# Performance work log

Hardware: AMD Instinct MI355X
Metric: run time of the kernel (lower is better)

The kernel has to match this reference:

```python
import jax, jax.numpy as jnp
import numpy as np

NUM_HEADS = 6
HEAD_SIZE = 64
N_EMBD = 384


def setup_inputs() -> dict:
    key = jax.random.key(0)
    ks = jax.random.split(key, 6)
    B, T, C = 4, 2048, N_EMBD
    D = NUM_HEADS * HEAD_SIZE  # 384
    x = jax.random.normal(ks[0], (B, T, C), dtype=jnp.float32)
    scale = 1.0 / np.sqrt(C)
    Wq = jax.random.normal(ks[1], (C, D), dtype=jnp.float32) * scale
    Wk = jax.random.normal(ks[2], (C, D), dtype=jnp.float32) * scale
    Wv = jax.random.normal(ks[3], (C, D), dtype=jnp.float32) * scale
    Wp = jax.random.normal(ks[4], (D, N_EMBD), dtype=jnp.float32) * scale
    bp = jnp.zeros((N_EMBD,), dtype=jnp.float32)
    return {"x": x, "Wq": Wq, "Wk": Wk, "Wv": Wv, "Wp": Wp, "bp": bp}


def reference(x, Wq, Wk, Wv, Wp, bp):
    B, T, C = x.shape
    H, Dh = NUM_HEADS, HEAD_SIZE
    # QKV projections (no bias), split into heads: [B, H, T, Dh]
    q = (x @ Wq).reshape(B, T, H, Dh).transpose(0, 2, 1, 3)
    k = (x @ Wk).reshape(B, T, H, Dh).transpose(0, 2, 1, 3)
    v = (x @ Wv).reshape(B, T, H, Dh).transpose(0, 2, 1, 3)
    # scaled dot-product scores [B, H, T, T]
    scores = jnp.einsum("bhqd,bhkd->bhqk", q, k) / jnp.sqrt(jnp.float32(Dh))
    causal = jnp.tril(jnp.ones((T, T), dtype=bool))
    scores = jnp.where(causal, scores, jnp.float32(-1e9))
    attn = jax.nn.softmax(scores, axis=-1)
    # dropout is identity at inference (Keras Dropout inactive outside training)
    out = jnp.einsum("bhqk,bhkd->bhqd", attn, v)
    out = out.transpose(0, 2, 1, 3).reshape(B, T, H * Dh)
    return out @ Wp + bp
```

## Files before the change

kernel.cpp:

```cpp
#include <hip/hip_runtime.h>
#include <hip/hip_bf16.h>

typedef __bf16 bf16x8 __attribute__((ext_vector_type(8)));
typedef float floatx4 __attribute__((ext_vector_type(4)));
typedef unsigned short us4 __attribute__((ext_vector_type(4)));
typedef unsigned short us8 __attribute__((ext_vector_type(8)));
typedef unsigned short ushort_t;

#define MFMA(a,b,c) __builtin_amdgcn_mfma_f32_16x16x32_bf16((a),(b),(c),0,0,0)


__device__ __forceinline__ ushort_t f2bf(float f){
  unsigned u = __builtin_bit_cast(unsigned, f);
  u = u + 0x7fffu + ((u>>16)&1u);
  return (ushort_t)(u>>16);
}

__device__ __forceinline__ us4 pack4(float4 a){
  us4 o;
  o[0]=f2bf(a.x); o[1]=f2bf(a.y); o[2]=f2bf(a.z); o[3]=f2bf(a.w);
  return o;
}

__device__ __forceinline__ us4 cvt4(floatx4 v){
  union { us4 s; __hip_bfloat162 h[2]; } u;
  float2 t;
  t.x=v[0]; t.y=v[1]; u.h[0]=__float22bfloat162_rn(t);
  t.x=v[2]; t.y=v[3]; u.h[1]=__float22bfloat162_rn(t);
  return u.s;
}

__global__ __launch_bounds__(256) void prep(
    const float* __restrict__ x,
    const float* __restrict__ w0, const float* __restrict__ w1,
    const float* __restrict__ w2, const float* __restrict__ w3,
    ushort_t* __restrict__ xb,
    ushort_t* __restrict__ wt_qkv, ushort_t* __restrict__ wt_p){
  __shared__ ushort_t tile[64][65];
  int bx = blockIdx.x;
  if (bx < 3072){
    int i = (bx*256 + threadIdx.x)*4;
    int row = i/384, col = i - row*384;
    float4 v = *(const float4*)(x + i);
    us4 o;
    o[0]=f2bf(v.x); o[1]=f2bf(v.y); o[2]=f2bf(v.z); o[3]=f2bf(v.w);
    *(us4*)(xb + ((row>>4)*48 + (col>>3))*128 + (row&15)*8 + (col&7)) = o;
    return;
  }
  int t6 = bx - 3072;
  int z = t6/36, rem = t6%36, by = rem/6, bxx = rem%6;
  const float* src; ushort_t* dst;
  if      (z==0){ src=w0; dst=wt_qkv;             }
  else if (z==1){ src=w1; dst=wt_qkv + 147456;    }
  else if (z==2){ src=w2; dst=wt_qkv + 2*147456;  }
  else          { src=w3; dst=wt_p;               }
  int r0 = by*64, c0 = bxx*64;
  int t = threadIdx.x, r = t>>2, cs = (t&3)*16;
  #pragma unroll
  for (int i=0;i<16;i++) tile[r][cs+i] = f2bf(src[(r0+r)*384 + c0+cs+i]);
  __syncthreads();
  int n = c0 + r, t16n = n>>4, rn = n&15;
  int k0 = r0 + cs;
  #pragma unroll
  for (int i=0;i<16;i++){
    int k = k0 + i;
    dst[(t16n*48 + (k>>3))*128 + rn*8 + (k&7)] = tile[cs+i][r];
  }
}

__global__ __launch_bounds__(64) void qkv_gemm(
    const ushort_t* __restrict__ x, const ushort_t* __restrict__ wt,
    ushort_t* __restrict__ qb, ushort_t* __restrict__ kb, ushort_t* __restrict__ vtb){
  __shared__ ushort_t tr[16*72];
  int lane = threadIdx.x&63, l15 = lane&15, quad = lane>>4;
  int mb = blockIdx.x*64, mt = blockIdx.x*4;
  int z  = blockIdx.y/6;
  int nt16 = (blockIdx.y - z*6)*4;
  int n0 = nt16*16;
  const ushort_t* wbase = wt + z*147456;
  floatx4 acc[4][4];
  #pragma unroll
  for (int qs=0;qs<4;qs++)
    #pragma unroll
    for (int nt=0;nt<4;nt++) acc[qs][nt]=(floatx4){0,0,0,0};
  #pragma unroll
  for (int kt=0; kt<12; kt++){
    bf16x8 a[4], b[4];
    #pragma unroll
    for (int qs=0; qs<4; qs++)
      a[qs] = *(const bf16x8*)(x + ((mt+qs)*48 + kt*4+quad)*128 + l15*8);
    #pragma unroll
    for (int nt=0; nt<4; nt++)
      b[nt] = *(const bf16x8*)(wbase + ((nt16+nt)*48 + kt*4+quad)*128 + l15*8);
    #pragma unroll
    for (int qs=0; qs<4; qs++)
      #pragma unroll
      for (int nt=0; nt<4; nt++)
        acc[qs][nt] = MFMA(a[qs], b[nt], acc[qs][nt]);
  }
  int h = n0>>6;
  if (z == 2){
    #pragma unroll
    for (int qs=0; qs<4; qs++){
      int rbase = mb + qs*16 + quad*4;
      int b_ = rbase >> 11, rr = rbase & 2047;
      int ct = rr>>3, e0 = rr&7;
      #pragma unroll
      for (int nt=0; nt<4; nt++){
        float4 v; v.x=acc[qs][nt][0]; v.y=acc[qs][nt][1];
                  v.z=acc[qs][nt][2]; v.w=acc[qs][nt][3];
        *(us4*)(vtb + ((b_*6+h)*1024 + nt*256 + ct)*128 + l15*8 + e0) = pack4(v);
      }
    }
  } else {
    float qscale = (z==0) ? 0.18033688011112042f : 1.0f;
    ushort_t* dstp = (z==0) ? qb : kb;
    #pragma unroll
    for (int qs=0; qs<4; qs++){
      int rbase = mb + qs*16;
      int b_ = rbase>>11, t16 = (rbase&2047)>>4;
      #pragma unroll
      for (int nt=0; nt<4; nt++)
        #pragma unroll
        for (int j=0; j<4; j++)
          tr[(quad*4+j)*72 + nt*16 + l15] = f2bf(acc[qs][nt][j]*qscale);
      us8 v0 = *(const us8*)(&tr[l15*72 + quad*8]);
      us8 v1 = *(const us8*)(&tr[l15*72 + (quad+4)*8]);
      int hbase = (b_*6+h)*1024 + t16*8;
      *(us8*)(dstp + (hbase + quad  )*128 + l15*8) = v0;
      *(us8*)(dstp + (hbase + quad+4)*128 + l15*8) = v1;
    }
  }
}

__device__ __forceinline__ void score(
    const bf16x8 (&kf)[4][2], bf16x8 qf0, bf16x8 qf1,
    ushort_t* slice, int qg, int kv0, bool diag, int l15, int quad){
  floatx4 s[4];
  #pragma unroll
  for (int nt=0; nt<4; nt++){
    floatx4 z = {0,0,0,0};
    z = MFMA(kf[nt][0], qf0, z);
    z = MFMA(kf[nt][1], qf1, z);
    s[nt] = z;
  }
  ushort_t* prow = slice + l15*72;
  if (diag){
    #pragma unroll
    for (int nt=0; nt<4; nt++){
      floatx4 p;
      #pragma unroll
      for (int r=0;r<4;r++){
        int kvg = kv0 + nt*16 + quad*4 + r;
        float sv = (kvg > qg) ? -1e30f : s[nt][r];
        p[r] = exp2f(sv);
      }
      *(us4*)(prow + nt*16 + quad*4) = cvt4(p);
    }
  } else {
    #pragma unroll
    for (int nt=0; nt<4; nt++){
      floatx4 p;
      #pragma unroll
      for (int r=0;r<4;r++) p[r] = exp2f(s[nt][r]);
      *(us4*)(prow + nt*16 + quad*4) = cvt4(p);
    }
  }
}

__device__ __forceinline__ void pv(
    const bf16x8 (&vf)[4][2], bf16x8 ones, ushort_t* slice,
    floatx4 (&o4)[4], floatx4& lsum, int l15, int quad){
  ushort_t* prow = slice + l15*72;
  bf16x8 pa0 = *(const bf16x8*)(prow + quad*8);
  bf16x8 pa1 = *(const bf16x8*)(prow + 32 + quad*8);
  #pragma unroll
  for (int nt=0; nt<4; nt++){
    o4[nt] = MFMA(pa0, vf[nt][0], o4[nt]);
    o4[nt] = MFMA(pa1, vf[nt][1], o4[nt]);
  }
  lsum = MFMA(pa0, ones, lsum);
  lsum = MFMA(pa1, ones, lsum);
}

__global__ __launch_bounds__(256,2) void attn(
    const ushort_t* __restrict__ qb, const ushort_t* __restrict__ kb,
    const ushort_t* __restrict__ vtb, ushort_t* __restrict__ ob){
  __shared__ float smem[9472];
  int bx = blockIdx.x;
  int hb = bx % 24;
  int p  = bx / 24;
  int tA = p, tB = 63 - p;
  int ktA = tA >> 1, ktB = tB >> 1;
  int h = hb % 6, b = hb / 6;
  int lane = threadIdx.x&63, w = threadIdx.x>>6, l15 = lane&15, quad = lane>>4;
  const ushort_t* qbase = qb  + (b*6+h)*131072;
  const ushort_t* kbase = kb  + (b*6+h)*131072;
  const ushort_t* vbase = vtb + (b*6+h)*131072;

  bf16x8 qfA[2][2], qfB[2][2];
  #pragma unroll
  for (int s=0; s<2; s++){
    const ushort_t* qpA = qbase + ((tA*2+s)*8 + quad)*128 + l15*8;
    qfA[s][0] = *(const bf16x8*)(qpA);
    qfA[s][1] = *(const bf16x8*)(qpA + 512);
    const ushort_t* qpB = qbase + ((tB*2+s)*8 + quad)*128 + l15*8;
    qfB[s][0] = *(const bf16x8*)(qpB);
    qfB[s][1] = *(const bf16x8*)(qpB + 512);
  }
  union { us8 u; bf16x8 v; } onesu;
  #pragma unroll
  for (int i=0;i<8;i++) onesu.u[i] = 0x3F80;
  bf16x8 ones = onesu.v;

  floatx4 oA[2][4], oB[2][4];
  floatx4 lsA[2], lsB[2];
  #pragma unroll
  for (int s=0;s<2;s++){
    lsA[s] = (floatx4){0,0,0,0};
    lsB[s] = (floatx4){0,0,0,0};
    #pragma unroll
    for (int i=0;i<4;i++){ oA[s][i]=(floatx4){0,0,0,0}; oB[s][i]=(floatx4){0,0,0,0}; }
  }

  ushort_t* s0 = (ushort_t*)smem + w*4608;
  ushort_t* s1 = s0 + 1152;
  ushort_t* s2 = s0 + 2304;
  ushort_t* s3 = s0 + 3456;
  int qA0 = tA*32, qB0 = tB*32;

  auto LOADK = [&](int t, bf16x8 (&kf_)[4][2]){
    #pragma unroll
    for (int nt=0; nt<4; nt++){
      const ushort_t* kp = kbase + ((t*4+nt)*8 + quad)*128 + l15*8;
      kf_[nt][0] = *(const bf16x8*)(kp);
      kf_[nt][1] = *(const bf16x8*)(kp + 512);
    }
  };
  auto LOADV = [&](int t, bf16x8 (&vf_)[4][2]){
    #pragma unroll
    for (int nt=0; nt<4; nt++){
      const ushort_t* vp = vbase + (nt*256 + t*8 + quad)*128 + l15*8;
      vf_[nt][0] = *(const bf16x8*)(vp);
      vf_[nt][1] = *(const bf16x8*)(vp + 512);
    }
  };

  bf16x8 kf[4][2], vf[4][2];
  LOADK(w, kf); LOADV(w, vf);

  for (int kt=w; kt<=ktB; kt+=4){
    int kv0 = kt*64;
    int ktn = (kt+4 <= ktB) ? kt+4 : ktB;
    bool diagB = (kt == ktB);
    bf16x8 kn[4][2], vn[4][2];
    score(kf, qfB[0][0],qfB[0][1], s0, qB0   +l15, kv0, diagB, l15, quad);
    score(kf, qfB[1][0],qfB[1][1], s1, qB0+16+l15, kv0, diagB, l15, quad);
    pv(vf, ones, s0, oB[0], lsB[0], l15, quad);
    if (kt <= ktA){
      bool diagA = (kt == ktA);
      score(kf, qfA[0][0],qfA[0][1], s2, qA0   +l15, kv0, diagA, l15, quad);
      pv(vf, ones, s1, oB[1], lsB[1], l15, quad);
      score(kf, qfA[1][0],qfA[1][1], s3, qA0+16+l15, kv0, diagA, l15, quad);
      LOADK(ktn, kn);
      pv(vf, ones, s2, oA[0], lsA[0], l15, quad);
      pv(vf, ones, s3, oA[1], lsA[1], l15, quad);
      LOADV(ktn, vn);
    } else {
      pv(vf, ones, s1, oB[1], lsB[1], l15, quad);
      LOADK(ktn, kn);
      LOADV(ktn, vn);
    }
    #pragma unroll
    for (int nt=0; nt<4; nt++){
      kf[nt][0]=kn[nt][0]; kf[nt][1]=kn[nt][1];
      vf[nt][0]=vn[nt][0]; vf[nt][1]=vn[nt][1];
    }
  }

  float* lsh = smem + 9216;
  if (l15==0){
    #pragma unroll
    for (int j=0;j<4;j++){
      lsh[w*64 +      quad*4 + j] = lsA[0][j];
      lsh[w*64 + 16 + quad*4 + j] = lsA[1][j];
      lsh[w*64 + 32 + quad*4 + j] = lsB[0][j];
      lsh[w*64 + 48 + quad*4 + j] = lsB[1][j];
    }
  }

  auto do_chunk = [&](const floatx4 (&oc)[4], int c, int grc){
    __syncthreads();
    #pragma unroll
    for (int j=0;j<4;j++){
      int r16 = quad*4 + j;
      #pragma unroll
      for (int nt=0;nt<4;nt++)
        smem[w*1088 + r16*68 + nt*16 + l15] = oc[nt][j];
    }
    __syncthreads();
    #pragma unroll
    for (int jj=0;jj<4;jj++){
      int r16 = w*4 + jj;
      float l = lsh[c*16+r16] + lsh[64+c*16+r16]
              + lsh[128+c*16+r16] + lsh[192+c*16+r16];
      float acc = smem[r16*68+lane] + smem[1088 + r16*68+lane]
                + smem[2176 + r16*68+lane] + smem[3264 + r16*68+lane];
      ob[((b*128 + grc)*48 + h*8 + (lane>>3))*128 + r16*8 + (lane&7)]
          = f2bf(acc/l);
    }
  };
  do_chunk(oA[0], 0, tA*2);
  do_chunk(oA[1], 1, tA*2+1);
  do_chunk(oB[0], 2, tB*2);
  do_chunk(oB[1], 3, tB*2+1);
}

__global__ __launch_bounds__(64) void proj_gemm(
    const ushort_t* __restrict__ a, const ushort_t* __restrict__ wpt,
    const float* __restrict__ bp, float* __restrict__ out){
  int lane = threadIdx.x&63, l15 = lane&15, quad = lane>>4;
  int mb = blockIdx.x*64, mt = blockIdx.x*4;
  int nb = blockIdx.y*64, nt16 = blockIdx.y*4;
  floatx4 acc[4][4];
  #pragma unroll
  for (int qs=0;qs<4;qs++)
    #pragma unroll
    for (int nt=0;nt<4;nt++) acc[qs][nt]=(floatx4){0,0,0,0};
  #pragma unroll
  for (int kt=0; kt<12; kt++){
    bf16x8 av[4], bv[4];
    #pragma unroll
    for (int qs=0; qs<4; qs++)
      av[qs] = *(const bf16x8*)(a + ((mt+qs)*48 + kt*4+quad)*128 + l15*8);
    #pragma unroll
    for (int nt=0; nt<4; nt++)
      bv[nt] = *(const bf16x8*)(wpt + ((nt16+nt)*48 + kt*4+quad)*128 + l15*8);
    #pragma unroll
    for (int qs=0; qs<4; qs++)
      #pragma unroll
      for (int nt=0; nt<4; nt++)
        acc[qs][nt] = MFMA(av[qs], bv[nt], acc[qs][nt]);
  }
  #pragma unroll
  for (int qs=0; qs<4; qs++){
    #pragma unroll
    for (int nt=0; nt<4; nt++){
      int c = nb + nt*16 + l15;
      float bias = bp[c];
      #pragma unroll
      for (int j=0; j<4; j++){
        int r = mb + qs*16 + quad*4 + j;
        out[r*384 + c] = acc[qs][nt][j] + bias;
      }
    }
  }
}

extern "C" void kernel_launch(void* const* d_in, const int* in_sizes, int n_in,
                              void* d_out, int out_size, void* d_ws, size_t ws_size,
                              hipStream_t stream){
  const float* x  = (const float*)d_in[0];
  const float* Wq = (const float*)d_in[1];
  const float* Wk = (const float*)d_in[2];
  const float* Wv = (const float*)d_in[3];
  const float* Wp = (const float*)d_in[4];
  const float* bp = (const float*)d_in[5];
  float* out = (float*)d_out;

  ushort_t* xb  = (ushort_t*)d_ws;
  ushort_t* wt  = xb  + 8192*384;
  ushort_t* wpt = wt  + 1152*384;
  ushort_t* qb  = wpt + 384*384;
  ushort_t* kb  = qb  + 8192*384;
  ushort_t* vtb = kb  + 8192*384;
  ushort_t* ab  = vtb + 8192*384;

  prep     <<<dim3(3216),   256, 0, stream>>>(x,Wq,Wk,Wv,Wp,xb,wt,wpt);
  qkv_gemm <<<dim3(128,18), 64,  0, stream>>>(xb, wt, qb, kb, vtb);
  attn     <<<dim3(768),    256, 0, stream>>>(qb, kb, vtb, ab);
  proj_gemm<<<dim3(128,6),  64,  0, stream>>>(ab, wpt, bp, out);
}
```

Measured before the change: 131.5 us.

## Share one K/V register buffer and split attention loop into two phases

Replaces the separate double-buffered K and V fragment arrays with a single shared register array. V is loaded after the score step and the next K after the PV step, which cuts register pressure. The loop is split into a phase handling both query tiles and a tail phase handling only tile B, which removes the per-iteration branch. In exchange, K/V loads are no longer prefetched a full iteration ahead, so load latency is more exposed and depends on occupancy gains to hide it.

```diff
diff --git a/kernel.cpp b/kernel.cpp
--- a/kernel.cpp
+++ b/kernel.cpp
@@ -229,53 +229,49 @@
   ushort_t* s3 = s0 + 3456;
   int qA0 = tA*32, qB0 = tB*32;
 
-  auto LOADK = [&](int t, bf16x8 (&kf_)[4][2]){
+  bf16x8 kv[4][2];
+  auto LOADK = [&](int t){
     #pragma unroll
     for (int nt=0; nt<4; nt++){
       const ushort_t* kp = kbase + ((t*4+nt)*8 + quad)*128 + l15*8;
-      kf_[nt][0] = *(const bf16x8*)(kp);
-      kf_[nt][1] = *(const bf16x8*)(kp + 512);
+      kv[nt][0] = *(const bf16x8*)(kp);
+      kv[nt][1] = *(const bf16x8*)(kp + 512);
     }
   };
-  auto LOADV = [&](int t, bf16x8 (&vf_)[4][2]){
+  auto LOADV = [&](int t){
     #pragma unroll
     for (int nt=0; nt<4; nt++){
       const ushort_t* vp = vbase + (nt*256 + t*8 + quad)*128 + l15*8;
-      vf_[nt][0] = *(const bf16x8*)(vp);
-      vf_[nt][1] = *(const bf16x8*)(vp + 512);
+      kv[nt][0] = *(const bf16x8*)(vp);
+      kv[nt][1] = *(const bf16x8*)(vp + 512);
     }
   };
 
-  bf16x8 kf[4][2], vf[4][2];
-  LOADK(w, kf); LOADV(w, vf);
-
-  for (int kt=w; kt<=ktB; kt+=4){
+  int kt = w;
+  LOADK(kt);
+  for (; kt <= ktA; kt += 4){
     int kv0 = kt*64;
-    int ktn = (kt+4 <= ktB) ? kt+4 : ktB;
+    bool diagA = (kt == ktA);
+    score(kv, qfB[0][0],qfB[0][1], s0, qB0   +l15, kv0, false, l15, quad);
+    score(kv, qfB[1][0],qfB[1][1], s1, qB0+16+l15, kv0, false, l15, quad);
+    score(kv, qfA[0][0],qfA[0][1], s2, qA0   +l15, kv0, diagA, l15, quad);
+    score(kv, qfA[1][0],qfA[1][1], s3, qA0+16+l15, kv0, diagA, l15, quad);
+    LOADV(kt);
+    pv(kv, ones, s0, oB[0], lsB[0], l15, quad);
+    pv(kv, ones, s1, oB[1], lsB[1], l15, quad);
+    pv(kv, ones, s2, oA[0], lsA[0], l15, quad);
+    pv(kv, ones, s3, oA[1], lsA[1], l15, quad);
+    LOADK((kt+4 <= ktB) ? kt+4 : ktB);
+  }
+  for (; kt <= ktB; kt += 4){
+    int kv0 = kt*64;
     bool diagB = (kt == ktB);
-    bf16x8 kn[4][2], vn[4][2];
-    score(kf, qfB[0][0],qfB[0][1], s0, qB0   +l15, kv0, diagB, l15, quad);
-    score(kf, qfB[1][0],qfB[1][1], s1, qB0+16+l15, kv0, diagB, l15, quad);
-    pv(vf, ones, s0, oB[0], lsB[0], l15, quad);
-    if (kt <= ktA){
-      bool diagA = (kt == ktA);
-      score(kf, qfA[0][0],qfA[0][1], s2, qA0   +l15, kv0, diagA, l15, quad);
-      pv(vf, ones, s1, oB[1], lsB[1], l15, quad);
-      score(kf, qfA[1][0],qfA[1][1], s3, qA0+16+l15, kv0, diagA, l15, quad);
-      LOADK(ktn, kn);
-      pv(vf, ones, s2, oA[0], lsA[0], l15, quad);
-      pv(vf, ones, s3, oA[1], lsA[1], l15, quad);
-      LOADV(ktn, vn);
-    } else {
-      pv(vf, ones, s1, oB[1], lsB[1], l15, quad);
-      LOADK(ktn, kn);
-      LOADV(ktn, vn);
-    }
-    #pragma unroll
-    for (int nt=0; nt<4; nt++){
-      kf[nt][0]=kn[nt][0]; kf[nt][1]=kn[nt][1];
-      vf[nt][0]=vn[nt][0]; vf[nt][1]=vn[nt][1];
-    }
+    score(kv, qfB[0][0],qfB[0][1], s0, qB0   +l15, kv0, diagB, l15, quad);
+    score(kv, qfB[1][0],qfB[1][1], s1, qB0+16+l15, kv0, diagB, l15, quad);
+    LOADV(kt);
+    pv(kv, ones, s0, oB[0], lsB[0], l15, quad);
+    pv(kv, ones, s1, oB[1], lsB[1], l15, quad);
+    LOADK((kt+4 <= ktB) ? kt+4 : ktB);
   }
 
   float* lsh = smem + 9216;
```

Measured after the change: 137.1 us. 4.2% more time.
